# Kernel optimization log

Hardware: AMD Instinct MI355X
Metric: run time of the kernel (lower is better)

## Reference

```python
import jax, jax.numpy as jnp
import numpy as np

PE_DIM = 64

def _layernorm(x, g, b, eps=1e-5):
    m = jnp.mean(x, -1, keepdims=True)
    v = jnp.mean((x - m) ** 2, -1, keepdims=True)
    return (x - m) * jax.lax.rsqrt(v + eps) * g + b

def _sinusoidal_pe(t, dim=PE_DIM):
    half = dim // 2
    freqs = jnp.exp(-jnp.log(10000.0) * jnp.arange(half) / half).astype(t.dtype)
    ang = t[..., None] * freqs  # [..., half]
    return jnp.concatenate([jnp.sin(ang), jnp.cos(ang)], -1)

def _bilinear(feats, b, t, x, y):
    # feats [B,Wl,H,W,D]; b,t int32 [B,Q,Wl,M] (b broadcastable); x,y in [0,1]
    # matches torch grid_sample(mode=bilinear, padding_mode=border, align_corners=False)
    H, W = feats.shape[2], feats.shape[3]
    px = x * W - 0.5
    py = y * H - 0.5
    x0 = jnp.floor(px); y0 = jnp.floor(py)
    wx = (px - x0)[..., None]; wy = (py - y0)[..., None]
    x0i = jnp.clip(x0.astype(jnp.int32), 0, W - 1)
    x1i = jnp.clip(x0.astype(jnp.int32) + 1, 0, W - 1)
    y0i = jnp.clip(y0.astype(jnp.int32), 0, H - 1)
    y1i = jnp.clip(y0.astype(jnp.int32) + 1, 0, H - 1)
    v00 = feats[b, t, y0i, x0i]  # [B,Q,Wl,M,D]
    v01 = feats[b, t, y0i, x1i]
    v10 = feats[b, t, y1i, x0i]
    v11 = feats[b, t, y1i, x1i]
    return (v00 * (1 - wy) * (1 - wx) + v01 * (1 - wy) * wx
            + v10 * wy * (1 - wx) + v11 * wy * wx)

def setup_inputs() -> dict:
    key = jax.random.key(0)
    ks = jax.random.split(key, 20)
    B, Q, Wl, H, W, D, M = 4, 300, 8, 64, 64, 256, 4
    s = 0.02
    inp = {
        'q': jax.random.normal(ks[0], (B, Q, D), jnp.float32),
        'kv_feats': jax.random.normal(ks[1], (B, Wl, H, W, D), jnp.float32),
        'kv_mask': jnp.zeros((B, Wl, H, W), jnp.bool_),
        'delta_sec': jax.random.normal(ks[2], (B, Q, Wl), jnp.float32),
        'w_ref': jax.random.normal(ks[3], (D, 2), jnp.float32) * s,
        'b_ref': jnp.zeros((2,), jnp.float32),
        'w_delta': jax.random.normal(ks[4], (2 * D, 3 * M), jnp.float32) * s,
        'b_delta': jnp.zeros((3 * M,), jnp.float32),
        'w_alpha': jax.random.normal(ks[5], (2 * D, M), jnp.float32) * s,
        'b_alpha': jnp.zeros((M,), jnp.float32),
        'lam': jnp.array(1.0, jnp.float32),
        'w_proj': jax.random.normal(ks[6], (D, D), jnp.float32) * s,
        'b_proj': jnp.zeros((D,), jnp.float32),
        'ln1_g': jnp.ones((D,), jnp.float32), 'ln1_b': jnp.zeros((D,), jnp.float32),
        'ln2_g': jnp.ones((D,), jnp.float32), 'ln2_b': jnp.zeros((D,), jnp.float32),
        'w_ffn1': jax.random.normal(ks[7], (D, 4 * D), jnp.float32) * s,
        'b_ffn1': jnp.zeros((4 * D,), jnp.float32),
        'w_ffn2': jax.random.normal(ks[8], (4 * D, D), jnp.float32) * s,
        'b_ffn2': jnp.zeros((D,), jnp.float32),
        'w_rel': jax.random.normal(ks[9], (PE_DIM, D), jnp.float32) * s,
        'b_rel': jnp.zeros((D,), jnp.float32),
    }
    return inp

def reference(q, kv_feats, kv_mask, delta_sec, w_ref, b_ref, w_delta, b_delta,
              w_alpha, b_alpha, lam, w_proj, b_proj, ln1_g, ln1_b, ln2_g, ln2_b,
              w_ffn1, b_ffn1, w_ffn2, b_ffn2, w_rel, b_rel):
    B, Q, D = q.shape
    Wl = kv_feats.shape[1]
    M = w_alpha.shape[1]

    qn = _layernorm(q, ln1_g, ln1_b)
    rel_feat = _sinusoidal_pe(delta_sec) @ w_rel + b_rel          # [B,Q,Wl,D]
    psi = jnp.concatenate([jnp.broadcast_to(qn[:, :, None, :], (B, Q, Wl, D)),
                           rel_feat], -1)                          # [B,Q,Wl,2D]

    delta = (psi @ w_delta + b_delta).reshape(B, Q, Wl, M, 3)
    logits = psi @ w_alpha + b_alpha                               # [B,Q,Wl,M]
    ref = jax.nn.sigmoid(qn @ w_ref + b_ref)                       # [B,Q,2]
    coords = ref[:, :, None, None, :] + jnp.tanh(delta[..., :2])   # [B,Q,Wl,M,2]
    coords = jnp.clip(coords, 0.0, 1.0)
    delta_t = jnp.tanh(delta[..., 2])                              # [B,Q,Wl,M]

    # mask features (mask==True -> invalid -> zero)
    feats = kv_feats * (~kv_mask)[..., None].astype(kv_feats.dtype)

    # temporal trilinear indices
    base = jnp.arange(Wl, dtype=q.dtype).reshape(1, 1, Wl, 1)
    target = base + delta_t
    t0f = jnp.clip(jnp.floor(target), 0, Wl - 1)
    t1f = jnp.clip(t0f + 1, 0, Wl - 1)
    alpha = (target - t0f)[..., None]
    t0 = t0f.astype(jnp.int32); t1 = t1f.astype(jnp.int32)

    bidx = jnp.arange(B, dtype=jnp.int32).reshape(B, 1, 1, 1)
    cx = coords[..., 0]; cy = coords[..., 1]
    s0 = _bilinear(feats, bidx, t0, cx, cy)                        # [B,Q,Wl,M,D]
    s1 = _bilinear(feats, bidx, t1, cx, cy)
    sampled = s0 * (1 - alpha) + s1 * alpha

    lam_sp = jax.nn.softplus(lam)
    weights = jax.nn.softmax(logits - lam_sp * jnp.abs(delta_sec)[..., None], axis=-1)
    agg = jnp.sum(weights[..., None] * sampled, axis=(2, 3))       # [B,Q,D]

    out = q + (agg @ w_proj + b_proj)
    h = _layernorm(out, ln2_g, ln2_b)
    ffn = jax.nn.gelu(h @ w_ffn1 + b_ffn1, approximate=False) @ w_ffn2 + b_ffn2
    return out + ffn
```

## Files before the change

kernel.cpp:

```cpp
#include <hip/hip_runtime.h>
#include <math.h>

#define Bn 4
#define Qn 300
#define WL 8
#define Hh 64
#define Ww 64
#define Dd 256
#define Mm 4

__device__ __forceinline__ float wave_reduce(float v) {
#pragma unroll
    for (int off = 32; off > 0; off >>= 1) v += __shfl_down(v, off, 64);
    return v;
}

__device__ __forceinline__ float block_reduce256(float v, float* lds) {
    v = wave_reduce(v);
    int lane = threadIdx.x & 63, wv = threadIdx.x >> 6;
    if (lane == 0) lds[wv] = v;
    __syncthreads();
    float r = lds[0] + lds[1] + lds[2] + lds[3];
    __syncthreads();
    return r;
}

__device__ __forceinline__ float lo16(unsigned u) { return __uint_as_float(u << 16); }
__device__ __forceinline__ float hi16(unsigned u) { return __uint_as_float(u & 0xffff0000u); }

__device__ __forceinline__ unsigned bfp(float a, float b) {
    unsigned ua = __float_as_uint(a); ua = (ua + 0x7fffu + ((ua >> 16) & 1u)) >> 16;
    unsigned ub = __float_as_uint(b); ub = (ub + 0x7fffu + ((ub >> 16) & 1u)) >> 16;
    return ua | (ub << 16);
}

__global__ void __launch_bounds__(256) k_prep(const float* __restrict__ wp,
                                              const float* __restrict__ wf1,
                                              const float* __restrict__ wf2,
                                              const float* __restrict__ w_rel,
                                              const float* __restrict__ dsec,
                                              const float* __restrict__ w_delta,
                                              const float* __restrict__ w_alpha,
                                              unsigned* __restrict__ pk,
                                              float* __restrict__ wrT,
                                              float* __restrict__ WcTg,
                                              float* __restrict__ peg) {
    int bid = blockIdx.x, t = threadIdx.x;
    if (bid < 1152) {
        int i = bid * 256 + t;
        if (i < 32768) {
            int p = i & 3, c = (i >> 2) & 255, g = i >> 10;
            pk[i] = bfp(wp[(g * 8 + 2 * p) * 256 + c], wp[(g * 8 + 2 * p + 1) * 256 + c]);
        } else if (i < 163840) {
            int i2 = i - 32768;
            int p = i2 & 3, c = (i2 >> 2) & 1023, g = i2 >> 12;
            pk[i] = bfp(wf1[(g * 8 + 2 * p) * 1024 + c], wf1[(g * 8 + 2 * p + 1) * 1024 + c]);
        } else {
            int i3 = i - 163840;
            int p = i3 & 3, c = (i3 >> 2) & 255, g = i3 >> 10;
            pk[i] = bfp(wf2[(g * 8 + 2 * p) * 256 + c], wf2[(g * 8 + 2 * p + 1) * 256 + c]);
        }
    } else if (bid < 1216) {
        int u = (bid - 1152) * 256 + t;
        int col = u >> 6, k = u & 63;
        wrT[u] = w_rel[k * 256 + col];
    } else if (bid < 1248) {
        int u = (bid - 1216) * 256 + t;
        int jj = u >> 9, k = u & 511;
        WcTg[u] = (jj < 12) ? w_delta[k * 12 + jj] : w_alpha[k * 4 + (jj - 12)];
    } else {
        int bq = bid - 1248;
        int wl = t >> 5, i = t & 31;
        float f = expf(-logf(10000.f) * (float)i * (1.f / 32.f));
        float a = dsec[bq * WL + wl] * f;
        peg[bq * 512 + wl * 64 + i] = sinf(a);
        peg[bq * 512 + wl * 64 + 32 + i] = cosf(a);
    }
}

__global__ void __launch_bounds__(256) k_mid(const float* __restrict__ q,
                                             const float* __restrict__ g1,
                                             const float* __restrict__ b1,
                                             const float* __restrict__ w_ref,
                                             const float* __restrict__ b_ref,
                                             const float* __restrict__ wrT,
                                             const float* __restrict__ WcTg,
                                             const float* __restrict__ peg,
                                             const float* __restrict__ b_rel,
                                             const float* __restrict__ b_delta,
                                             const float* __restrict__ b_alpha,
                                             const unsigned char* __restrict__ mask,
                                             unsigned* __restrict__ prm2) {
    __shared__ float lds[4];
    __shared__ float sref[2];
    __shared__ float sqn[256];
    __shared__ float relS[8][260];
    __shared__ float qpart[8][16];
    __shared__ float rp[8][8][16];
    __shared__ float res[8][16];

    int bq = blockIdx.x, t = threadIdx.x;

    float x = q[bq * Dd + t];
    float m = block_reduce256(x, lds) * (1.f / Dd);
    float dx = x - m;
    float v = block_reduce256(dx * dx, lds) * (1.f / Dd);
    float y = dx * rsqrtf(v + 1e-5f) * g1[t] + b1[t];
    sqn[t] = y;

    float s0 = block_reduce256(y * w_ref[t * 2 + 0], lds);
    float s1 = block_reduce256(y * w_ref[t * 2 + 1], lds);
    if (t == 0) {
        sref[0] = 1.f / (1.f + expf(-(s0 + b_ref[0])));
        sref[1] = 1.f / (1.f + expf(-(s1 + b_ref[1])));
    }

    float wr[64];
    {
        const float4* w4 = (const float4*)&wrT[t * 64];
#pragma unroll
        for (int i = 0; i < 16; i++) {
            float4 vv = w4[i];
            wr[4 * i] = vv.x; wr[4 * i + 1] = vv.y; wr[4 * i + 2] = vv.z; wr[4 * i + 3] = vv.w;
        }
    }

    {
        const float* pg = peg + bq * 512;
        float brl = b_rel[t];
#pragma unroll
        for (int wl = 0; wl < WL; wl++) {
            const float4* p4 = (const float4*)(pg + wl * 64);
            float r = brl;
#pragma unroll
            for (int k4 = 0; k4 < 16; k4++) {
                float4 p = p4[k4];
                r += p.x * wr[4 * k4] + p.y * wr[4 * k4 + 1]
                   + p.z * wr[4 * k4 + 2] + p.w * wr[4 * k4 + 3];
            }
            relS[wl][t] = r;
        }
    }
    __syncthreads();

    {
        int chunk = t >> 4, jj = t & 15;
        float w[32];
        const float4* wg = (const float4*)&WcTg[jj * 512 + chunk * 32];
#pragma unroll
        for (int i = 0; i < 8; i++) {
            float4 vv = wg[i];
            w[4 * i] = vv.x; w[4 * i + 1] = vv.y; w[4 * i + 2] = vv.z; w[4 * i + 3] = vv.w;
        }
        if (chunk < 8) {
            const float4* a4 = (const float4*)&sqn[chunk * 32];
            float s = 0.f;
#pragma unroll
            for (int ii = 0; ii < 8; ii++) {
                int i = (ii + chunk) & 7;
                float4 a = a4[i];
                s += a.x * w[4 * i] + a.y * w[4 * i + 1] + a.z * w[4 * i + 2] + a.w * w[4 * i + 3];
            }
            qpart[chunk][jj] = s;
        } else {
            int ch = chunk - 8;
#pragma unroll
            for (int wl = 0; wl < WL; wl++) {
                const float4* a4 = (const float4*)&relS[wl][ch * 32];
                float s = 0.f;
#pragma unroll
                for (int ii = 0; ii < 8; ii++) {
                    int i = (ii + ch) & 7;
                    float4 a = a4[i];
                    s += a.x * w[4 * i] + a.y * w[4 * i + 1] + a.z * w[4 * i + 2] + a.w * w[4 * i + 3];
                }
                rp[wl][ch][jj] = s;
            }
        }
    }
    __syncthreads();
    if (t < 128) {
        int wl = t >> 4, jj = t & 15;
        float s = (jj < 12) ? b_delta[jj] : b_alpha[jj - 12];
#pragma unroll
        for (int c = 0; c < 8; c++) s += qpart[c][jj] + rp[wl][c][jj];
        res[wl][jj] = s;
    }
    __syncthreads();

    if (t < 32) {
        int wl = t >> 2, mm = t & 3;
        float l0 = res[wl][12], l1 = res[wl][13], l2 = res[wl][14], l3 = res[wl][15];
        float mx = fmaxf(fmaxf(l0, l1), fmaxf(l2, l3));
        float inv = 1.f / (expf(l0 - mx) + expf(l1 - mx) + expf(l2 - mx) + expf(l3 - mx));
        float wgt = expf(res[wl][12 + mm] - mx) * inv;

        float cx = fminf(fmaxf(sref[0] + tanhf(res[wl][mm * 3 + 0]), 0.f), 1.f);
        float cy = fminf(fmaxf(sref[1] + tanhf(res[wl][mm * 3 + 1]), 0.f), 1.f);
        float tgt = (float)wl + tanhf(res[wl][mm * 3 + 2]);
        float t0f = fminf(fmaxf(floorf(tgt), 0.f), (float)(WL - 1));
        float t1f = fminf(t0f + 1.f, (float)(WL - 1));
        float alpha = tgt - t0f;
        float px = cx * (float)Ww - 0.5f, py = cy * (float)Hh - 0.5f;
        float fx = floorf(px), fy = floorf(py);
        float wx = px - fx, wy = py - fy;
        int X0 = (int)fminf(fmaxf(fx, 0.f), (float)(Ww - 1));
        int X1 = (int)fminf(fmaxf(fx + 1.f, 0.f), (float)(Ww - 1));
        int Y0 = (int)fminf(fmaxf(fy, 0.f), (float)(Hh - 1));
        int Y1 = (int)fminf(fmaxf(fy + 1.f, 0.f), (float)(Hh - 1));
        int T0 = (int)t0f, T1 = (int)t1f;

        float w00 = (1.f - wy) * (1.f - wx), w01 = (1.f - wy) * wx;
        float w10 = wy * (1.f - wx), w11 = wy * wx;
        float wt0 = wgt * (1.f - alpha), wt1 = wgt * alpha;

        int b = bq / Qn;
        int base0 = (b * WL + T0) * Hh;
        int base1 = (b * WL + T1) * Hh;
        int i00 = (base0 + Y0) * Ww + X0, i01 = (base0 + Y0) * Ww + X1;
        int i10 = (base0 + Y1) * Ww + X0, i11 = (base0 + Y1) * Ww + X1;
        int j00 = (base1 + Y0) * Ww + X0, j01 = (base1 + Y0) * Ww + X1;
        int j10 = (base1 + Y1) * Ww + X0, j11 = (base1 + Y1) * Ww + X1;

        unsigned* rec = prm2 + (unsigned)(bq * 32 + t) * 16;
        rec[0] = __float_as_uint(wt0 * w00 * (mask[i00] ? 0.f : 1.f));
        rec[1] = __float_as_uint(wt0 * w01 * (mask[i01] ? 0.f : 1.f));
        rec[2] = __float_as_uint(wt0 * w10 * (mask[i10] ? 0.f : 1.f));
        rec[3] = __float_as_uint(wt0 * w11 * (mask[i11] ? 0.f : 1.f));
        rec[4] = __float_as_uint(wt1 * w00 * (mask[j00] ? 0.f : 1.f));
        rec[5] = __float_as_uint(wt1 * w01 * (mask[j01] ? 0.f : 1.f));
        rec[6] = __float_as_uint(wt1 * w10 * (mask[j10] ? 0.f : 1.f));
        rec[7] = __float_as_uint(wt1 * w11 * (mask[j11] ? 0.f : 1.f));
        rec[8] = i00; rec[9] = i01; rec[10] = i10; rec[11] = i11;
        rec[12] = j00; rec[13] = j01; rec[14] = j10; rec[15] = j11;
    }
}

__global__ void __launch_bounds__(512) k_gather(const float* __restrict__ feats,
                                                const unsigned* __restrict__ prm2,
                                                float* __restrict__ agg) {
    __shared__ unsigned P[32 * 16];
    __shared__ float part[8][256];
    int bq = blockIdx.x, t = threadIdx.x;
    int l = t & 63, j = t >> 6;
    P[t] = prm2[(unsigned)bq * 512 + t];
    __syncthreads();
    const float4* f4 = (const float4*)feats;
    float4 acc = {0.f, 0.f, 0.f, 0.f};
#pragma unroll
    for (int p = 0; p < 4; p++) {
        const unsigned* rec = &P[(j * 4 + p) * 16];
#pragma unroll
        for (int cn = 0; cn < 8; cn++) {
            float w = __uint_as_float(rec[cn]);
            size_t idx = rec[8 + cn];
            float4 v = f4[idx * 64 + l];
            acc.x += w * v.x; acc.y += w * v.y; acc.z += w * v.z; acc.w += w * v.w;
        }
    }
    ((float4*)&part[j][0])[l] = acc;
    __syncthreads();
    if (t < 256) {
        float s = part[0][t] + part[1][t] + part[2][t] + part[3][t]
                + part[4][t] + part[5][t] + part[6][t] + part[7][t];
        agg[(size_t)bq * Dd + t] = s;
    }
}

template<int R>
__device__ __forceinline__ void out_body(int row0,
        const float* __restrict__ q, const float* __restrict__ agg,
        const unsigned* __restrict__ pkP, const float* __restrict__ b_proj,
        const float* __restrict__ g2, const float* __restrict__ b2,
        const unsigned* __restrict__ pkF1, const float* __restrict__ b_ffn1,
        const unsigned* __restrict__ pkF2, const float* __restrict__ b_ffn2,
        float* __restrict__ out,
        float* sA, float* sO, float* sH, float* sF, float* sP, float* sRed) {
    int t = threadIdx.x;

    for (int u = t; u < 256 * R; u += 1024) {
        int r = u >> 8, cc = u & 255;
        sA[r * 256 + cc] = agg[(size_t)(row0 + r) * Dd + cc];
    }
    __syncthreads();

    if (t < 256) {
        int j = t >> 6, cq = t & 63;
        float acc[R][4];
#pragma unroll
        for (int r = 0; r < R; r++)
#pragma unroll
            for (int cc = 0; cc < 4; cc++) acc[r][cc] = 0.f;
#pragma unroll 2
        for (int gg = 0; gg < 8; gg++) {
            int g = j * 8 + gg;
            uint4 wv[4];
#pragma unroll
            for (int cc = 0; cc < 4; cc++)
                wv[cc] = *(const uint4*)&pkP[((g * 256) + cq + 64 * cc) * 4];
            float4 ha[R], hb[R];
#pragma unroll
            for (int r = 0; r < R; r++) {
                ha[r] = ((const float4*)&sA[r * 256])[g * 2];
                hb[r] = ((const float4*)&sA[r * 256])[g * 2 + 1];
            }
#pragma unroll
            for (int cc = 0; cc < 4; cc++) {
                float w0 = lo16(wv[cc].x), w1 = hi16(wv[cc].x);
                float w2 = lo16(wv[cc].y), w3 = hi16(wv[cc].y);
                float w4 = lo16(wv[cc].z), w5 = hi16(wv[cc].z);
                float w6 = lo16(wv[cc].w), w7 = hi16(wv[cc].w);
#pragma unroll
                for (int r = 0; r < R; r++) {
                    acc[r][cc] += ha[r].x * w0 + ha[r].y * w1 + ha[r].z * w2 + ha[r].w * w3
                                + hb[r].x * w4 + hb[r].y * w5 + hb[r].z * w6 + hb[r].w * w7;
                }
            }
        }
#pragma unroll
        for (int r = 0; r < R; r++)
#pragma unroll
            for (int cc = 0; cc < 4; cc++)
                sP[(j * 5 + r) * 256 + cq + 64 * cc] = acc[r][cc];
    }
    __syncthreads();

    for (int u = t; u < 256 * R; u += 1024) {
        int r = u >> 8, cc = u & 255;
        float o = sP[(0 * 5 + r) * 256 + cc] + sP[(1 * 5 + r) * 256 + cc]
                + sP[(2 * 5 + r) * 256 + cc] + sP[(3 * 5 + r) * 256 + cc]
                + q[(size_t)(row0 + r) * Dd + cc] + b_proj[cc];
        sO[r * 256 + cc] = o;
    }
    __syncthreads();

    {
        int wv = t >> 6, l = t & 63;
        if (wv < R) {
            float4 v = ((const float4*)&sO[wv * 256])[l];
            float s = v.x + v.y + v.z + v.w;
            s = __shfl(wave_reduce(s), 0, 64);
            float mean = s * (1.f / 256.f);
            float d0 = v.x - mean, d1 = v.y - mean, d2 = v.z - mean, d3 = v.w - mean;
            float ss = d0 * d0 + d1 * d1 + d2 * d2 + d3 * d3;
            ss = __shfl(wave_reduce(ss), 0, 64);
            float rstd = rsqrtf(ss * (1.f / 256.f) + 1e-5f);
            if (l == 0) { sRed[wv * 2] = mean; sRed[wv * 2 + 1] = rstd; }
        }
    }
    __syncthreads();
    for (int u = t; u < 256 * R; u += 1024) {
        int r = u >> 8, cc = u & 255;
        sH[r * 256 + cc] = (sO[r * 256 + cc] - sRed[r * 2]) * sRed[r * 2 + 1] * g2[cc] + b2[cc];
    }
    __syncthreads();

    if (t < 256) {
        float f[R][4];
#pragma unroll
        for (int r = 0; r < R; r++)
#pragma unroll
            for (int cc = 0; cc < 4; cc++) f[r][cc] = 0.f;
#pragma unroll 2
        for (int g = 0; g < 32; g++) {
            uint4 wv[4];
#pragma unroll
            for (int cc = 0; cc < 4; cc++)
                wv[cc] = *(const uint4*)&pkF1[((g * 1024) + t + 256 * cc) * 4];
            float4 ha[R], hb[R];
#pragma unroll
            for (int r = 0; r < R; r++) {
                ha[r] = ((const float4*)&sH[r * 256])[g * 2];
                hb[r] = ((const float4*)&sH[r * 256])[g * 2 + 1];
            }
#pragma unroll
            for (int cc = 0; cc < 4; cc++) {
                float w0 = lo16(wv[cc].x), w1 = hi16(wv[cc].x);
                float w2 = lo16(wv[cc].y), w3 = hi16(wv[cc].y);
                float w4 = lo16(wv[cc].z), w5 = hi16(wv[cc].z);
                float w6 = lo16(wv[cc].w), w7 = hi16(wv[cc].w);
#pragma unroll
                for (int r = 0; r < R; r++) {
                    f[r][cc] += ha[r].x * w0 + ha[r].y * w1 + ha[r].z * w2 + ha[r].w * w3
                              + hb[r].x * w4 + hb[r].y * w5 + hb[r].z * w6 + hb[r].w * w7;
                }
            }
        }
#pragma unroll
        for (int cc = 0; cc < 4; cc++) {
            int col = t + 256 * cc;
            float bf = b_ffn1[col];
#pragma unroll
            for (int r = 0; r < R; r++) {
                float xx = f[r][cc] + bf;
                sF[r * 1024 + col] = 0.5f * xx * (1.f + erff(xx * 0.70710678118654752f));
            }
        }
    }
    __syncthreads();

    if (t < 256) {
        int j = t >> 6, cq = t & 63;
        float acc[R][4];
#pragma unroll
        for (int r = 0; r < R; r++)
#pragma unroll
            for (int cc = 0; cc < 4; cc++) acc[r][cc] = 0.f;
#pragma unroll 2
        for (int gg = 0; gg < 32; gg++) {
            int g = j * 32 + gg;
            uint4 wv[4];
#pragma unroll
            for (int cc = 0; cc < 4; cc++)
                wv[cc] = *(const uint4*)&pkF2[((g * 256) + cq + 64 * cc) * 4];
            float4 ha[R], hb[R];
#pragma unroll
            for (int r = 0; r < R; r++) {
                ha[r] = ((const float4*)&sF[r * 1024])[g * 2];
                hb[r] = ((const float4*)&sF[r * 1024])[g * 2 + 1];
            }
#pragma unroll
            for (int cc = 0; cc < 4; cc++) {
                float w0 = lo16(wv[cc].x), w1 = hi16(wv[cc].x);
                float w2 = lo16(wv[cc].y), w3 = hi16(wv[cc].y);
                float w4 = lo16(wv[cc].z), w5 = hi16(wv[cc].z);
                float w6 = lo16(wv[cc].w), w7 = hi16(wv[cc].w);
#pragma unroll
                for (int r = 0; r < R; r++) {
                    acc[r][cc] += ha[r].x * w0 + ha[r].y * w1 + ha[r].z * w2 + ha[r].w * w3
                                + hb[r].x * w4 + hb[r].y * w5 + hb[r].z * w6 + hb[r].w * w7;
                }
            }
        }
#pragma unroll
        for (int r = 0; r < R; r++)
#pragma unroll
            for (int cc = 0; cc < 4; cc++)
                sP[(j * 5 + r) * 256 + cq + 64 * cc] = acc[r][cc];
    }
    __syncthreads();

    for (int u = t; u < 256 * R; u += 1024) {
        int r = u >> 8, cc = u & 255;
        float s = sP[(0 * 5 + r) * 256 + cc] + sP[(1 * 5 + r) * 256 + cc]
                + sP[(2 * 5 + r) * 256 + cc] + sP[(3 * 5 + r) * 256 + cc];
        out[(size_t)(row0 + r) * Dd + cc] = sO[r * 256 + cc] + s + b_ffn2[cc];
    }
}

__global__ void __launch_bounds__(1024) k_out(const float* __restrict__ q,
                                              const float* __restrict__ agg,
                                              const unsigned* __restrict__ pkP,
                                              const float* __restrict__ b_proj,
                                              const float* __restrict__ g2,
                                              const float* __restrict__ b2,
                                              const unsigned* __restrict__ pkF1,
                                              const float* __restrict__ b_ffn1,
                                              const unsigned* __restrict__ pkF2,
                                              const float* __restrict__ b_ffn2,
                                              float* __restrict__ out) {
    __shared__ float sA[5 * 256];
    __shared__ float sO[5 * 256];
    __shared__ float sH[5 * 256];
    __shared__ float sF[5 * 1024];
    __shared__ float sP[4 * 5 * 256];
    __shared__ float sRed[16];
    __shared__ float pad[8192];
    if (b_ffn2 == nullptr) pad[threadIdx.x] = 0.f;

    int bid = blockIdx.x;
    if (bid < 176) {
        out_body<5>(bid * 5, q, agg, pkP, b_proj, g2, b2, pkF1, b_ffn1, pkF2, b_ffn2,
                    out, sA, sO, sH, sF, sP, sRed);
    } else {
        out_body<4>(880 + (bid - 176) * 4, q, agg, pkP, b_proj, g2, b2, pkF1, b_ffn1,
                    pkF2, b_ffn2, out, sA, sO, sH, sF, sP, sRed);
    }
}

extern "C" void kernel_launch(void* const* d_in, const int* in_sizes, int n_in,
                              void* d_out, int out_size, void* d_ws, size_t ws_size,
                              hipStream_t stream) {
    const float* q        = (const float*)d_in[0];
    const float* kv_feats = (const float*)d_in[1];
    const unsigned char* kv_mask = (const unsigned char*)d_in[2];
    const float* delta_sec= (const float*)d_in[3];
    const float* w_ref    = (const float*)d_in[4];
    const float* b_ref    = (const float*)d_in[5];
    const float* w_delta  = (const float*)d_in[6];
    const float* b_delta  = (const float*)d_in[7];
    const float* w_alpha  = (const float*)d_in[8];
    const float* b_alpha  = (const float*)d_in[9];
    const float* w_proj   = (const float*)d_in[11];
    const float* b_proj   = (const float*)d_in[12];
    const float* ln1_g    = (const float*)d_in[13];
    const float* ln1_b    = (const float*)d_in[14];
    const float* ln2_g    = (const float*)d_in[15];
    const float* ln2_b    = (const float*)d_in[16];
    const float* w_ffn1   = (const float*)d_in[17];
    const float* b_ffn1   = (const float*)d_in[18];
    const float* w_ffn2   = (const float*)d_in[19];
    const float* b_ffn2   = (const float*)d_in[20];
    const float* w_rel    = (const float*)d_in[21];
    const float* b_rel    = (const float*)d_in[22];
    float* out = (float*)d_out;

    unsigned* pk   = (unsigned*)d_ws;
    unsigned* pkP  = pk;
    unsigned* pkF1 = pk + 32768;
    unsigned* pkF2 = pk + 163840;
    float*    wrT  = (float*)(pk + 294912);
    float*    WcTg = wrT + 16384;
    float*    peg  = WcTg + 8192;
    unsigned* prm2 = (unsigned*)(peg + 614400);
    float*    agg  = (float*)(prm2 + 614400);

    const int BQ = Bn * Qn;
    k_prep<<<dim3(1248 + BQ), dim3(256), 0, stream>>>(w_proj, w_ffn1, w_ffn2, w_rel,
                                                      delta_sec, w_delta, w_alpha,
                                                      pk, wrT, WcTg, peg);
    k_mid<<<dim3(BQ), dim3(256), 0, stream>>>(q, ln1_g, ln1_b, w_ref, b_ref,
                                              wrT, WcTg, peg, b_rel,
                                              b_delta, b_alpha, kv_mask, prm2);
    k_gather<<<dim3(BQ), dim3(512), 0, stream>>>(kv_feats, prm2, agg);
    k_out<<<dim3(256), dim3(1024), 0, stream>>>(q, agg, pkP, b_proj, ln2_g, ln2_b,
                                                pkF1, b_ffn1, pkF2, b_ffn2, out);
}
```

Measured before the change: 314.0 us.

## Fuse prep positional encoding, mid and gather kernels; widen out-kernel matmul threads

Folds the sinusoidal positional-encoding computation, the per-query offset and weight computation, and the feature gather into one 512-thread kernel. Sampling records now stay in shared memory, so the peg and prm2 global buffers and one launch are no longer needed. The out kernel's projection and FFN matmuls now use all 1024 threads, one column each, where previously 256 threads each computed four columns. The cost is more idle threads in the LayerNorm phase of the fused kernel and higher shared-memory and register use per block, which may lower occupancy.

```diff
diff --git a/kernel.cpp b/kernel.cpp
--- a/kernel.cpp
+++ b/kernel.cpp
@@ -15,12 +15,12 @@
     return v;
 }
 
-__device__ __forceinline__ float block_reduce256(float v, float* lds) {
+__device__ __forceinline__ float block_reduce512(float v, float* lds) {
     v = wave_reduce(v);
     int lane = threadIdx.x & 63, wv = threadIdx.x >> 6;
     if (lane == 0) lds[wv] = v;
     __syncthreads();
-    float r = lds[0] + lds[1] + lds[2] + lds[3];
+    float r = lds[0] + lds[1] + lds[2] + lds[3] + lds[4] + lds[5] + lds[6] + lds[7];
     __syncthreads();
     return r;
 }
@@ -38,13 +38,11 @@
                                               const float* __restrict__ wf1,
                                               const float* __restrict__ wf2,
                                               const float* __restrict__ w_rel,
-                                              const float* __restrict__ dsec,
                                               const float* __restrict__ w_delta,
                                               const float* __restrict__ w_alpha,
                                               unsigned* __restrict__ pk,
                                               float* __restrict__ wrT,
-                                              float* __restrict__ WcTg,
-                                              float* __restrict__ peg) {
+                                              float* __restrict__ WcTg) {
     int bid = blockIdx.x, t = threadIdx.x;
     if (bid < 1152) {
         int i = bid * 256 + t;
@@ -64,73 +62,80 @@
         int u = (bid - 1152) * 256 + t;
         int col = u >> 6, k = u & 63;
         wrT[u] = w_rel[k * 256 + col];
-    } else if (bid < 1248) {
+    } else {
         int u = (bid - 1216) * 256 + t;
         int jj = u >> 9, k = u & 511;
         WcTg[u] = (jj < 12) ? w_delta[k * 12 + jj] : w_alpha[k * 4 + (jj - 12)];
-    } else {
-        int bq = bid - 1248;
-        int wl = t >> 5, i = t & 31;
-        float f = expf(-logf(10000.f) * (float)i * (1.f / 32.f));
-        float a = dsec[bq * WL + wl] * f;
-        peg[bq * 512 + wl * 64 + i] = sinf(a);
-        peg[bq * 512 + wl * 64 + 32 + i] = cosf(a);
-    }
-}
-
-__global__ void __launch_bounds__(256) k_mid(const float* __restrict__ q,
-                                             const float* __restrict__ g1,
-                                             const float* __restrict__ b1,
-                                             const float* __restrict__ w_ref,
-                                             const float* __restrict__ b_ref,
-                                             const float* __restrict__ wrT,
-                                             const float* __restrict__ WcTg,
-                                             const float* __restrict__ peg,
-                                             const float* __restrict__ b_rel,
-                                             const float* __restrict__ b_delta,
-                                             const float* __restrict__ b_alpha,
-                                             const unsigned char* __restrict__ mask,
-                                             unsigned* __restrict__ prm2) {
-    __shared__ float lds[4];
+    }
+}
+
+__global__ void __launch_bounds__(512) k_fused(const float* __restrict__ q,
+                                               const float* __restrict__ g1,
+                                               const float* __restrict__ b1,
+                                               const float* __restrict__ w_ref,
+                                               const float* __restrict__ b_ref,
+                                               const float* __restrict__ dsec,
+                                               const float* __restrict__ wrT,
+                                               const float* __restrict__ WcTg,
+                                               const float* __restrict__ b_rel,
+                                               const float* __restrict__ b_delta,
+                                               const float* __restrict__ b_alpha,
+                                               const unsigned char* __restrict__ mask,
+                                               const float* __restrict__ feats,
+                                               float* __restrict__ agg) {
+    __shared__ float lds[8];
     __shared__ float sref[2];
     __shared__ float sqn[256];
+    __shared__ float pe[8][64];
     __shared__ float relS[8][260];
     __shared__ float qpart[8][16];
     __shared__ float rp[8][8][16];
     __shared__ float res[8][16];
+    __shared__ unsigned recS[32 * 16];
+    __shared__ float part[8][256];
 
     int bq = blockIdx.x, t = threadIdx.x;
 
-    float x = q[bq * Dd + t];
-    float m = block_reduce256(x, lds) * (1.f / Dd);
+    float x = (t < 256) ? q[bq * Dd + t] : 0.f;
+    float m = block_reduce512(x, lds) * (1.f / Dd);
     float dx = x - m;
-    float v = block_reduce256(dx * dx, lds) * (1.f / Dd);
-    float y = dx * rsqrtf(v + 1e-5f) * g1[t] + b1[t];
-    sqn[t] = y;
-
-    float s0 = block_reduce256(y * w_ref[t * 2 + 0], lds);
-    float s1 = block_reduce256(y * w_ref[t * 2 + 1], lds);
+    float v = block_reduce512((t < 256) ? dx * dx : 0.f, lds) * (1.f / Dd);
+    float y = 0.f;
+    if (t < 256) {
+        y = dx * rsqrtf(v + 1e-5f) * g1[t] + b1[t];
+        sqn[t] = y;
+    }
+
+    float s0 = block_reduce512((t < 256) ? y * w_ref[t * 2 + 0] : 0.f, lds);
+    float s1 = block_reduce512((t < 256) ? y * w_ref[t * 2 + 1] : 0.f, lds);
     if (t == 0) {
         sref[0] = 1.f / (1.f + expf(-(s0 + b_ref[0])));
         sref[1] = 1.f / (1.f + expf(-(s1 + b_ref[1])));
     }
 
-    float wr[64];
-    {
-        const float4* w4 = (const float4*)&wrT[t * 64];
+    if (t < 256) {
+        int wl = t >> 5, i = t & 31;
+        float f = expf(-logf(10000.f) * (float)i * (1.f / 32.f));
+        float a = dsec[bq * WL + wl] * f;
+        pe[wl][i] = sinf(a);
+        pe[wl][i + 32] = cosf(a);
+    }
+    __syncthreads();
+
+    {
+        int col = t & 255, half = t >> 8;
+        float wr[64];
+        const float4* w4 = (const float4*)&wrT[col * 64];
 #pragma unroll
         for (int i = 0; i < 16; i++) {
             float4 vv = w4[i];
             wr[4 * i] = vv.x; wr[4 * i + 1] = vv.y; wr[4 * i + 2] = vv.z; wr[4 * i + 3] = vv.w;
         }
-    }
-
-    {
-        const float* pg = peg + bq * 512;
-        float brl = b_rel[t];
-#pragma unroll
-        for (int wl = 0; wl < WL; wl++) {
-            const float4* p4 = (const float4*)(pg + wl * 64);
+        float brl = b_rel[col];
+#pragma unroll
+        for (int w8 = 0; w8 < 4; w8++) {
+            int wl = half * 4 + w8;
+            const float4* p4 = (const float4*)&pe[wl][0];
             float r = brl;
 #pragma unroll
             for (int k4 = 0; k4 < 16; k4++) {
@@ -138,12 +143,12 @@
                 r += p.x * wr[4 * k4] + p.y * wr[4 * k4 + 1]
                    + p.z * wr[4 * k4 + 2] + p.w * wr[4 * k4 + 3];
             }
-            relS[wl][t] = r;
-        }
-    }
-    __syncthreads();
-
-    {
+            relS[wl][col] = r;
+        }
+    }
+    __syncthreads();
+
+    if (t < 256) {
         int chunk = t >> 4, jj = t & 15;
         float w[32];
         const float4* wg = (const float4*)&WcTg[jj * 512 + chunk * 32];
@@ -222,7 +227,7 @@
         int j00 = (base1 + Y0) * Ww + X0, j01 = (base1 + Y0) * Ww + X1;
         int j10 = (base1 + Y1) * Ww + X0, j11 = (base1 + Y1) * Ww + X1;
 
-        unsigned* rec = prm2 + (unsigned)(bq * 32 + t) * 16;
+        unsigned* rec = &recS[t * 16];
         rec[0] = __float_as_uint(wt0 * w00 * (mask[i00] ? 0.f : 1.f));
         rec[1] = __float_as_uint(wt0 * w01 * (mask[i01] ? 0.f : 1.f));
         rec[2] = __float_as_uint(wt0 * w10 * (mask[i10] ? 0.f : 1.f));
@@ -234,31 +239,25 @@
         rec[8] = i00; rec[9] = i01; rec[10] = i10; rec[11] = i11;
         rec[12] = j00; rec[13] = j01; rec[14] = j10; rec[15] = j11;
     }
-}
-
-__global__ void __launch_bounds__(512) k_gather(const float* __restrict__ feats,
-                                                const unsigned* __restrict__ prm2,
-                                                float* __restrict__ agg) {
-    __shared__ unsigned P[32 * 16];
-    __shared__ float part[8][256];
-    int bq = blockIdx.x, t = threadIdx.x;
-    int l = t & 63, j = t >> 6;
-    P[t] = prm2[(unsigned)bq * 512 + t];
-    __syncthreads();
-    const float4* f4 = (const float4*)feats;
-    float4 acc = {0.f, 0.f, 0.f, 0.f};
-#pragma unroll
-    for (int p = 0; p < 4; p++) {
-        const unsigned* rec = &P[(j * 4 + p) * 16];
-#pragma unroll
-        for (int cn = 0; cn < 8; cn++) {
-            float w = __uint_as_float(rec[cn]);
-            size_t idx = rec[8 + cn];
-            float4 v = f4[idx * 64 + l];
-            acc.x += w * v.x; acc.y += w * v.y; acc.z += w * v.z; acc.w += w * v.w;
-        }
-    }
-    ((float4*)&part[j][0])[l] = acc;
+    __syncthreads();
+
+    {
+        int l = t & 63, j = t >> 6;
+        const float4* f4 = (const float4*)feats;
+        float4 acc = {0.f, 0.f, 0.f, 0.f};
+#pragma unroll
+        for (int p = 0; p < 4; p++) {
+            const unsigned* rec = &recS[(j * 4 + p) * 16];
+#pragma unroll
+            for (int cn = 0; cn < 8; cn++) {
+                float w = __uint_as_float(rec[cn]);
+                size_t idx = rec[8 + cn];
+                float4 vv = f4[idx * 64 + l];
+                acc.x += w * vv.x; acc.y += w * vv.y; acc.z += w * vv.z; acc.w += w * vv.w;
+            }
+        }
+        ((float4*)&part[j][0])[l] = acc;
+    }
     __syncthreads();
     if (t < 256) {
         float s = part[0][t] + part[1][t] + part[2][t] + part[3][t]
@@ -277,6 +276,7 @@
         float* __restrict__ out,
         float* sA, float* sO, float* sH, float* sF, float* sP, float* sRed) {
     int t = threadIdx.x;
+    int c = t & 255, j = t >> 8;
 
     for (int u = t; u < 256 * R; u += 1024) {
         int r = u >> 8, cc = u & 255;
@@ -284,44 +284,26 @@
     }
     __syncthreads();
 
-    if (t < 256) {
-        int j = t >> 6, cq = t & 63;
-        float acc[R][4];
-#pragma unroll
-        for (int r = 0; r < R; r++)
-#pragma unroll
-            for (int cc = 0; cc < 4; cc++) acc[r][cc] = 0.f;
+    {
+        float acc[R];
+#pragma unroll
+        for (int r = 0; r < R; r++) acc[r] = 0.f;
 #pragma unroll 2
         for (int gg = 0; gg < 8; gg++) {
             int g = j * 8 + gg;
-            uint4 wv[4];
-#pragma unroll
-            for (int cc = 0; cc < 4; cc++)
-                wv[cc] = *(const uint4*)&pkP[((g * 256) + cq + 64 * cc) * 4];
-            float4 ha[R], hb[R];
+            uint4 wv = *(const uint4*)&pkP[((unsigned)(g * 256 + c)) * 4];
+            float w0 = lo16(wv.x), w1 = hi16(wv.x), w2 = lo16(wv.y), w3 = hi16(wv.y);
+            float w4 = lo16(wv.z), w5 = hi16(wv.z), w6 = lo16(wv.w), w7 = hi16(wv.w);
 #pragma unroll
             for (int r = 0; r < R; r++) {
-                ha[r] = ((const float4*)&sA[r * 256])[g * 2];
-                hb[r] = ((const float4*)&sA[r * 256])[g * 2 + 1];
-            }
-#pragma unroll
-            for (int cc = 0; cc < 4; cc++) {
-                float w0 = lo16(wv[cc].x), w1 = hi16(wv[cc].x);
-                float w2 = lo16(wv[cc].y), w3 = hi16(wv[cc].y);
-                float w4 = lo16(wv[cc].z), w5 = hi16(wv[cc].z);
-                float w6 = lo16(wv[cc].w), w7 = hi16(wv[cc].w);
-#pragma unroll
-                for (int r = 0; r < R; r++) {
-                    acc[r][cc] += ha[r].x * w0 + ha[r].y * w1 + ha[r].z * w2 + ha[r].w * w3
-                                + hb[r].x * w4 + hb[r].y * w5 + hb[r].z * w6 + hb[r].w * w7;
-                }
-            }
-        }
-#pragma unroll
-        for (int r = 0; r < R; r++)
-#pragma unroll
-            for (int cc = 0; cc < 4; cc++)
-                sP[(j * 5 + r) * 256 + cq + 64 * cc] = acc[r][cc];
+                float4 ha = ((const float4*)&sA[r * 256])[g * 2];
+                float4 hb = ((const float4*)&sA[r * 256])[g * 2 + 1];
+                acc[r] += ha.x * w0 + ha.y * w1 + ha.z * w2 + ha.w * w3
+                        + hb.x * w4 + hb.y * w5 + hb.z * w6 + hb.w * w7;
+            }
+        }
+#pragma unroll
+        for (int r = 0; r < R; r++) sP[(j * 5 + r) * 256 + c] = acc[r];
     }
     __syncthreads();
 
@@ -355,88 +337,52 @@
     }
     __syncthreads();
 
-    if (t < 256) {
-        float f[R][4];
-#pragma unroll
-        for (int r = 0; r < R; r++)
-#pragma unroll
-            for (int cc = 0; cc < 4; cc++) f[r][cc] = 0.f;
+    {
+        float f[R];
+#pragma unroll
+        for (int r = 0; r < R; r++) f[r] = 0.f;
 #pragma unroll 2
         for (int g = 0; g < 32; g++) {
-            uint4 wv[4];
-#pragma unroll
-            for (int cc = 0; cc < 4; cc++)
-                wv[cc] = *(const uint4*)&pkF1[((g * 1024) + t + 256 * cc) * 4];
-            float4 ha[R], hb[R];
+            uint4 wv = *(const uint4*)&pkF1[((unsigned)(g * 1024 + t)) * 4];
+            float w0 = lo16(wv.x), w1 = hi16(wv.x), w2 = lo16(wv.y), w3 = hi16(wv.y);
+            float w4 = lo16(wv.z), w5 = hi16(wv.z), w6 = lo16(wv.w), w7 = hi16(wv.w);
 #pragma unroll
             for (int r = 0; r < R; r++) {
-                ha[r] = ((const float4*)&sH[r * 256])[g * 2];
-                hb[r] = ((const float4*)&sH[r * 256])[g * 2 + 1];
-            }
-#pragma unroll
-            for (int cc = 0; cc < 4; cc++) {
-                float w0 = lo16(wv[cc].x), w1 = hi16(wv[cc].x);
-                float w2 = lo16(wv[cc].y), w3 = hi16(wv[cc].y);
-                float w4 = lo16(wv[cc].z), w5 = hi16(wv[cc].z);
-                float w6 = lo16(wv[cc].w), w7 = hi16(wv[cc].w);
-#pragma unroll
-                for (int r = 0; r < R; r++) {
-                    f[r][cc] += ha[r].x * w0 + ha[r].y * w1 + ha[r].z * w2 + ha[r].w * w3
-                              + hb[r].x * w4 + hb[r].y * w5 + hb[r].z * w6 + hb[r].w * w7;
-                }
-            }
-        }
-#pragma unroll
-        for (int cc = 0; cc < 4; cc++) {
-            int col = t + 256 * cc;
-            float bf = b_ffn1[col];
-#pragma unroll
-            for (int r = 0; r < R; r++) {
-                float xx = f[r][cc] + bf;
-                sF[r * 1024 + col] = 0.5f * xx * (1.f + erff(xx * 0.70710678118654752f));
-            }
-        }
-    }
-    __syncthreads();
-
-    if (t < 256) {
-        int j = t >> 6, cq = t & 63;
-        float acc[R][4];
-#pragma unroll
-        for (int r = 0; r < R; r++)
-#pragma unroll
-            for (int cc = 0; cc < 4; cc++) acc[r][cc] = 0.f;
+                float4 ha = ((const float4*)&sH[r * 256])[g * 2];
+                float4 hb = ((const float4*)&sH[r * 256])[g * 2 + 1];
+                f[r] += ha.x * w0 + ha.y * w1 + ha.z * w2 + ha.w * w3
+                      + hb.x * w4 + hb.y * w5 + hb.z * w6 + hb.w * w7;
+            }
+        }
+        float bf = b_ffn1[t];
+#pragma unroll
+        for (int r = 0; r < R; r++) {
+            float xx = f[r] + bf;
+            sF[r * 1024 + t] = 0.5f * xx * (1.f + erff(xx * 0.70710678118654752f));
+        }
+    }
+    __syncthreads();
+
+    {
+        float acc[R];
+#pragma unroll
+        for (int r = 0; r < R; r++) acc[r] = 0.f;
 #pragma unroll 2
         for (int gg = 0; gg < 32; gg++) {
             int g = j * 32 + gg;
-            uint4 wv[4];
-#pragma unroll
-            for (int cc = 0; cc < 4; cc++)
-                wv[cc] = *(const uint4*)&pkF2[((g * 256) + cq + 64 * cc) * 4];
-            float4 ha[R], hb[R];
+            uint4 wv = *(const uint4*)&pkF2[((unsigned)(g * 256 + c)) * 4];
+            float w0 = lo16(wv.x), w1 = hi16(wv.x), w2 = lo16(wv.y), w3 = hi16(wv.y);
+            float w4 = lo16(wv.z), w5 = hi16(wv.z), w6 = lo16(wv.w), w7 = hi16(wv.w);
 #pragma unroll
             for (int r = 0; r < R; r++) {
-                ha[r] = ((const float4*)&sF[r * 1024])[g * 2];
-                hb[r] = ((const float4*)&sF[r * 1024])[g * 2 + 1];
-            }
-#pragma unroll
-            for (int cc = 0; cc < 4; cc++) {
-                float w0 = lo16(wv[cc].x), w1 = hi16(wv[cc].x);
-                float w2 = lo16(wv[cc].y), w3 = hi16(wv[cc].y);
-                float w4 = lo16(wv[cc].z), w5 = hi16(wv[cc].z);
-                float w6 = lo16(wv[cc].w), w7 = hi16(wv[cc].w);
-#pragma unroll
-                for (int r = 0; r < R; r++) {
-                    acc[r][cc] += ha[r].x * w0 + ha[r].y * w1 + ha[r].z * w2 + ha[r].w * w3
-                                + hb[r].x * w4 + hb[r].y * w5 + hb[r].z * w6 + hb[r].w * w7;
-                }
-            }
-        }
-#pragma unroll
-        for (int r = 0; r < R; r++)
-#pragma unroll
-            for (int cc = 0; cc < 4; cc++)
-                sP[(j * 5 + r) * 256 + cq + 64 * cc] = acc[r][cc];
+                float4 ha = ((const float4*)&sF[r * 1024])[g * 2];
+                float4 hb = ((const float4*)&sF[r * 1024])[g * 2 + 1];
+                acc[r] += ha.x * w0 + ha.y * w1 + ha.z * w2 + ha.w * w3
+                        + hb.x * w4 + hb.y * w5 + hb.z * w6 + hb.w * w7;
+            }
+        }
+#pragma unroll
+        for (int r = 0; r < R; r++) sP[(j * 5 + r) * 256 + c] = acc[r];
     }
     __syncthreads();
 
@@ -511,18 +457,14 @@
     unsigned* pkF2 = pk + 163840;
     float*    wrT  = (float*)(pk + 294912);
     float*    WcTg = wrT + 16384;
-    float*    peg  = WcTg + 8192;
-    unsigned* prm2 = (unsigned*)(peg + 614400);
-    float*    agg  = (float*)(prm2 + 614400);
+    float*    agg  = WcTg + 8192;
 
     const int BQ = Bn * Qn;
-    k_prep<<<dim3(1248 + BQ), dim3(256), 0, stream>>>(w_proj, w_ffn1, w_ffn2, w_rel,
-                                                      delta_sec, w_delta, w_alpha,
-                                                      pk, wrT, WcTg, peg);
-    k_mid<<<dim3(BQ), dim3(256), 0, stream>>>(q, ln1_g, ln1_b, w_ref, b_ref,
-                                              wrT, WcTg, peg, b_rel,
-                                              b_delta, b_alpha, kv_mask, prm2);
-    k_gather<<<dim3(BQ), dim3(512), 0, stream>>>(kv_feats, prm2, agg);
+    k_prep<<<dim3(1248), dim3(256), 0, stream>>>(w_proj, w_ffn1, w_ffn2, w_rel,
+                                                 w_delta, w_alpha, pk, wrT, WcTg);
+    k_fused<<<dim3(BQ), dim3(512), 0, stream>>>(q, ln1_g, ln1_b, w_ref, b_ref, delta_sec,
+                                                wrT, WcTg, b_rel, b_delta, b_alpha,
+                                                kv_mask, kv_feats, agg);
     k_out<<<dim3(256), dim3(1024), 0, stream>>>(q, agg, pkP, b_proj, ln2_g, ln2_b,
                                                 pkF1, b_ffn1, pkF2, b_ffn2, out);
 }
```

Result: slower. 355.9 us (+13.3%).
